# Kernel tuning notes

Hardware: AMD Instinct MI355X
Metric: run time of the kernel (lower is better)

## Reference

```python
import jax, jax.numpy as jnp
import numpy as np

NH = 12      # config.n_head
LEVEL = 2    # config.level -> Lmin = 4


def setup_inputs() -> dict:
    key = jax.random.key(0)
    ks = jax.random.split(key, 10)
    B, T, C = 1, 2048, 768
    hs = C // NH
    s = 0.02
    return {
        'x':   jax.random.normal(ks[0], (B, T, C), jnp.float32),
        'Wq':  jax.random.normal(ks[1], (C, C), jnp.float32) * s,
        'Wk':  jax.random.normal(ks[2], (C, C), jnp.float32) * s,
        'Wv':  jax.random.normal(ks[3], (C, C), jnp.float32) * s,
        'Wks': jax.random.normal(ks[4], (hs * hs, hs), jnp.float32) * s,
        'bks': jax.random.normal(ks[5], (hs,), jnp.float32) * s,
        'Wvs': jax.random.normal(ks[6], (hs * hs, hs), jnp.float32) * s,
        'bvs': jax.random.normal(ks[7], (hs,), jnp.float32) * s,
        'Wc':  jax.random.normal(ks[8], (C, C), jnp.float32) * s,
        'bc':  jax.random.normal(ks[9], (C,), jnp.float32) * s,
    }


def reference(x, Wq, Wk, Wv, Wks, bks, Wvs, bvs, Wc, bc):
    B, T, C = x.shape
    hs = C // NH
    Lmin = 2 ** LEVEL
    levelmax = int(np.log2(T))          # T is a power of two -> no ragged tails per level
    scale = hs ** -0.5

    # fla LinearAttention preprocess: bias-free projections + elu feature map (phi = elu+1)
    q = (jax.nn.elu(x @ Wq) + 1.0).reshape(B, T, NH, hs)
    k = (jax.nn.elu(x @ Wk) + 1.0).reshape(B, T, NH, hs)
    v = (x @ Wv).reshape(B, T, NH, hs)

    # per-position linear-attn state increments phi(k) v^T  [B,T,H,hs,hs]
    kv = jnp.einsum('bthi,bthj->bthij', k, v).reshape(B, T, NH, hs * hs)

    # tail features: running state within each block of Lmin (fused_recurrent final states
    # over the ragged per-position tail segments [t - t%Lmin, t])
    tail_feat = jnp.cumsum(kv.reshape(B, T // Lmin, Lmin, NH, hs * hs), axis=2)
    tail_feat = tail_feat.reshape(B, T, NH, hs * hs)

    # hierarchical set features: dyadic block sums at levels LEVEL..levelmax
    cur = kv.reshape(B, T // Lmin, Lmin, NH, hs * hs).sum(axis=2)
    feats, ends = [], []
    for l in range(LEVEL, levelmax + 1):
        n = T // (2 ** l)
        feats.append(cur)
        ends.append(np.arange(1, n + 1) * (2 ** l))   # exclusive end index of each set
        if n >= 2:
            cur = cur.reshape(B, n // 2, 2, NH, hs * hs).sum(axis=2)
    set_feat = jnp.concatenate(feats, axis=1)          # [B, S, H, hs*hs], S = 1023
    ends = np.concatenate(ends)                        # [S]
    mask = ends[None, :] <= (np.arange(T) + 1)[:, None]  # [T, S] causal set mask

    # k_mapping / v_mapping: Linear(hs^2 -> hs)
    K = set_feat @ Wks + bks        # [B,S,H,hs]
    V = set_feat @ Wvs + bvs
    K_tail = tail_feat @ Wks + bks  # [B,T,H,hs]
    V_tail = tail_feat @ Wvs + bvs

    logits = jnp.einsum('bthd,bshd->bhts', q, K) * scale      # [B,H,T,S]
    logits = jnp.where(mask[None, None], logits, jnp.float32(-1e30))
    tail_logit = jnp.einsum('bthd,bthd->bht', q, K_tail) * scale  # [B,H,T]
    att = jax.nn.softmax(jnp.concatenate([logits, tail_logit[..., None]], axis=-1), axis=-1)

    out = jnp.einsum('bhts,bshd->bhtd', att[..., :-1], V)
    out = out + att[..., -1:] * V_tail.transpose(0, 2, 1, 3)  # [B,H,T,hs]
    out = out.transpose(0, 2, 1, 3).reshape(B, T, C)
    return out @ Wc + bc
```

## Files before the change

### kernel.cpp

```cpp
#include <hip/hip_runtime.h>
#include <cstdint>

#define NHEAD 12
#define TLEN 2048
#define CDIM 768
#define NSETS 1023

typedef __attribute__((ext_vector_type(8))) _Float16 half8;
typedef __attribute__((ext_vector_type(2))) __fp16 fp16x2;
typedef __attribute__((ext_vector_type(8))) short short8;
typedef __attribute__((ext_vector_type(8))) unsigned short u16x8;
typedef __attribute__((ext_vector_type(4))) float f32x4;

#define SOFTMAX_SCL 0.18033688011112042f

__device__ __forceinline__ float elu1(float x) { return x > 0.f ? x + 1.f : __expf(x); }

__device__ __forceinline__ unsigned pack2_bf16_trunc(float a, float b) {
    unsigned ua = __float_as_uint(a), ub = __float_as_uint(b);
    return __builtin_amdgcn_perm(ub, ua, 0x07060302);
}
__device__ __forceinline__ unsigned pack2_bf16_rne(float a, float b) {
    unsigned ua = __float_as_uint(a), ub = __float_as_uint(b);
    ua = ua + 0x7fff + ((ua >> 16) & 1);
    ub = ub + 0x7fff + ((ub >> 16) & 1);
    return (ub & 0xffff0000u) | (ua >> 16);
}
__device__ __forceinline__ unsigned short bf16_hi_trunc(float a) {
    return (unsigned short)(__float_as_uint(a) >> 16);
}
__device__ __forceinline__ unsigned short bf16_lo_trunc(float a) {
    unsigned ua = __float_as_uint(a);
    float r = a - __uint_as_float(ua & 0xffff0000u);
    return (unsigned short)(__float_as_uint(r) >> 16);
}
__device__ __forceinline__ unsigned short bf16_rne(float a) {
    unsigned ua = __float_as_uint(a);
    ua = ua + 0x7fff + ((ua >> 16) & 1);
    return (unsigned short)(ua >> 16);
}
__device__ __forceinline__ short8 mk_short8(const unsigned* u) {
    union { unsigned w[4]; short8 s; } x;
    x.w[0] = u[0]; x.w[1] = u[1]; x.w[2] = u[2]; x.w[3] = u[3];
    return x.s;
}
__device__ __forceinline__ short8 as_s8(u16x8 v) {
    union { u16x8 u; short8 s; } x; x.u = v; return x.s;
}
__device__ __forceinline__ void split8_bf16(const float* f, short8& hi, short8& lo) {
    unsigned hp[4], lp[4];
    #pragma unroll
    for (int p = 0; p < 4; ++p) {
        float a = f[2 * p], b = f[2 * p + 1];
        unsigned ua = __float_as_uint(a), ub = __float_as_uint(b);
        hp[p] = __builtin_amdgcn_perm(ub, ua, 0x07060302);
        float ra = a - __uint_as_float(ua & 0xffff0000u);
        float rb = b - __uint_as_float(ub & 0xffff0000u);
        lp[p] = pack2_bf16_trunc(ra, rb);
    }
    hi = mk_short8(hp); lo = mk_short8(lp);
}
__device__ __forceinline__ void split8_f16(const float* f, half8& hi, half8& lo) {
    union { fp16x2 h2[4]; half8 h8; } uh, ul;
    #pragma unroll
    for (int jp = 0; jp < 4; ++jp) {
        float a = f[2 * jp], b = f[2 * jp + 1];
        fp16x2 hh = __builtin_amdgcn_cvt_pkrtz(a, b);
        uh.h2[jp] = hh;
        ul.h2[jp] = __builtin_amdgcn_cvt_pkrtz(a - (float)hh[0], b - (float)hh[1]);
    }
    hi = uh.h8; lo = ul.h8;
}

__global__ __launch_bounds__(256) void prep_all(
    const float* __restrict__ Wq, const float* __restrict__ Wk,
    const float* __restrict__ Wv, const float* __restrict__ Wc4,
    const float* __restrict__ Wks, const float* __restrict__ Wvs,
    const float* __restrict__ x,
    _Float16* __restrict__ blobQKV, _Float16* __restrict__ blobC,
    _Float16* __restrict__ Wblob,
    _Float16* __restrict__ xhi, _Float16* __restrict__ xlo)
{
    const int g = blockIdx.x;
    const int tid = threadIdx.x;
    if (g < 9216) {
        const int sel = g / 2304;
        const float* W = sel == 0 ? Wq : (sel == 1 ? Wk : (sel == 2 ? Wv : Wc4));
        _Float16* blob = (sel < 3) ? (blobQKV + (size_t)sel * 589824) : blobC;
        const int idx = (g % 2304) * 256 + tid;
        const int k = idx / 768, n = idx % 768;
        const int i = k >> 5, kl = k & 31;
        const int quad = kl >> 3, j = kl & 7;
        const int nsg = n >> 4, lane15 = n & 15;
        const int lane = quad * 16 + lane15;
        blob[((size_t)(i * 48 + nsg) * 64 + lane) * 8 + j] = (_Float16)W[idx];
    } else if (g < 9216 + 2048) {
        const int idx = (g - 9216) * 256 + tid;
        const int kk = idx >> 7, n = idx & 127;
        float f = (n < 64) ? Wks[(size_t)kk * 64 + n] : Wvs[(size_t)kk * 64 + (n - 64)];
        const int i = kk >> 6, kl = kk & 63;
        const int ks = kl >> 5, quad = (kl >> 3) & 3, j = kl & 7;
        const int nsg = n >> 4, lane15 = n & 15;
        const int lane = quad * 16 + lane15;
        const size_t off = ((size_t)(((i * 2 + ks) * 8 + nsg)) * 64 + lane) * 8 + j;
        Wblob[off] = (_Float16)f;
    } else {
        const int p = (g - 11264) * 256 + tid;
        const int lane = p & 63, frag = p >> 6;
        const int m16 = frag / 24, k32 = frag - m16 * 24;
        const int row = m16 * 16 + (lane & 15);
        const int col = k32 * 32 + (lane >> 4) * 8;
        float f[8];
        *(float4*)&f[0] = *(const float4*)&x[(size_t)row * CDIM + col];
        *(float4*)&f[4] = *(const float4*)&x[(size_t)row * CDIM + col + 4];
        half8 h, l;
        split8_f16(f, h, l);
        *(half8*)&xhi[(size_t)p * 8] = h;
        *(half8*)&xlo[(size_t)p * 8] = l;
    }
}

template<int QKV>
__global__ __launch_bounds__(256, 3) void gemm_frag(
    const _Float16* __restrict__ Ahi, const _Float16* __restrict__ Alo,
    const _Float16* __restrict__ Bblobs, const float* __restrict__ bias,
    float* __restrict__ outq, unsigned* __restrict__ kdup,
    _Float16* __restrict__ v16)
{
    const int nbx = QKV ? 18 : 6;
    const int cpx = QKV ? 72 : 24;
    int bid = blockIdx.x;
    bid = (bid & 7) * cpx + (bid >> 3);
    const int by  = bid / nbx;
    const int bxg = bid % nbx;
    const int which = QKV ? bxg / 6 : 0;
    const int bxm   = QKV ? bxg % 6 : bxg;
    const half8* __restrict__ Bc = (const half8*)(Bblobs + (size_t)which * 589824);

    const int tid = threadIdx.x;
    const int wave = tid >> 6, lane = tid & 63;
    const int lane15 = lane & 15, quad = lane >> 4;
    const int m16b = by * 4;
    const int nsg0 = bxm * 8 + wave * 2;

    const half8* __restrict__ Ah = (const half8*)Ahi;
    const half8* __restrict__ Al = (const half8*)Alo;

    f32x4 acc[4][2];
    #pragma unroll
    for (int ms = 0; ms < 4; ++ms) {
        acc[ms][0] = (f32x4){0.f, 0.f, 0.f, 0.f};
        acc[ms][1] = (f32x4){0.f, 0.f, 0.f, 0.f};
    }

    const size_t aBase = ((size_t)m16b * 24) * 64 + lane;
    const size_t bBase = (size_t)nsg0 * 64 + lane;

    half8 bb[2], ah[4], al[4];
    bb[0] = Bc[bBase];
    bb[1] = Bc[bBase + 64];
    #pragma unroll
    for (int ms = 0; ms < 4; ++ms) {
        ah[ms] = Ah[aBase + (size_t)ms * (24 * 64)];
        al[ms] = Al[aBase + (size_t)ms * (24 * 64)];
    }

    for (int k32 = 0; k32 < 24; ++k32) {
        half8 bbn[2], ahn[4], aln[4];
        const bool more = (k32 + 1) < 24;
        if (more) {
            const size_t bo = bBase + (size_t)(k32 + 1) * (48 * 64);
            bbn[0] = Bc[bo]; bbn[1] = Bc[bo + 64];
            #pragma unroll
            for (int ms = 0; ms < 4; ++ms) {
                const size_t ao = aBase + (size_t)(k32 + 1) * 64 + (size_t)ms * (24 * 64);
                ahn[ms] = Ah[ao]; aln[ms] = Al[ao];
            }
        }
        #pragma unroll
        for (int ms = 0; ms < 4; ++ms) {
            acc[ms][0] = __builtin_amdgcn_mfma_f32_16x16x32_f16(ah[ms], bb[0], acc[ms][0], 0, 0, 0);
            acc[ms][1] = __builtin_amdgcn_mfma_f32_16x16x32_f16(ah[ms], bb[1], acc[ms][1], 0, 0, 0);
            acc[ms][0] = __builtin_amdgcn_mfma_f32_16x16x32_f16(al[ms], bb[0], acc[ms][0], 0, 0, 0);
            acc[ms][1] = __builtin_amdgcn_mfma_f32_16x16x32_f16(al[ms], bb[1], acc[ms][1], 0, 0, 0);
        }
        if (more) {
            bb[0] = bbn[0]; bb[1] = bbn[1];
            #pragma unroll
            for (int ms = 0; ms < 4; ++ms) { ah[ms] = ahn[ms]; al[ms] = aln[ms]; }
        }
    }

    #pragma unroll
    for (int ms = 0; ms < 4; ++ms)
        #pragma unroll
        for (int nb = 0; nb < 2; ++nb) {
            const int coln = (nsg0 + nb) * 16 + lane15;
            #pragma unroll
            for (int r = 0; r < 4; ++r) {
                const int row = m16b * 16 + ms * 16 + quad * 4 + r;
                float vv = acc[ms][nb][r];
                if (!QKV) {
                    outq[(size_t)row * CDIM + coln] = vv + bias[coln];
                } else if (which == 0) {
                    outq[(size_t)row * CDIM + coln] = elu1(vv);
                } else if (which == 1) {
                    float e = elu1(vv);
                    union { fp16x2 h; unsigned u; } cc;
                    cc.h = __builtin_amdgcn_cvt_pkrtz(e, e);
                    kdup[(size_t)row * CDIM + coln] = cc.u;
                } else {
                    union { fp16x2 h; _Float16 f2[2]; } cc;
                    cc.h = __builtin_amdgcn_cvt_pkrtz(vv, vv);
                    v16[(size_t)row * CDIM + coln] = cc.f2[0];
                }
            }
        }
}

__global__ __launch_bounds__(256, 2) void map_f16(
    const unsigned* __restrict__ kdup, const _Float16* __restrict__ v16,
    const _Float16* __restrict__ Wblob,
    float* __restrict__ kkv, float* __restrict__ vvv)
{
    __shared__ unsigned kU[64][65];

    const int tid = threadIdx.x;
    const int p0 = blockIdx.x * 64;
    const int wave = tid >> 6, lane = tid & 63;
    const int lane15 = lane & 15, quad = lane >> 4;

    {
        const int row = tid >> 2, cb = (tid & 3) * 16;
        const unsigned* src = &kdup[(size_t)(p0 + row) * 64 + cb];
        uint4 a0 = *(const uint4*)(src + 0);
        uint4 a1 = *(const uint4*)(src + 4);
        uint4 a2 = *(const uint4*)(src + 8);
        uint4 a3 = *(const uint4*)(src + 12);
        *(uint4*)&kU[row][cb + 0]  = a0;
        *(uint4*)&kU[row][cb + 4]  = a1;
        *(uint4*)&kU[row][cb + 8]  = a2;
        *(uint4*)&kU[row][cb + 12] = a3;
    }

    half8 vrh[4][2];
    #pragma unroll
    for (int mh = 0; mh < 4; ++mh) {
        const size_t pbase = (size_t)(p0 + mh * 16 + lane15) * 64;
        #pragma unroll
        for (int ks = 0; ks < 2; ++ks)
            vrh[mh][ks] = *(const half8*)&v16[pbase + ks * 32 + quad * 8];
    }
    __syncthreads();

    const half8* __restrict__ Wc = (const half8*)Wblob;

    f32x4 acc[4][2];
    #pragma unroll
    for (int mh = 0; mh < 4; ++mh)
        #pragma unroll
        for (int nsl = 0; nsl < 2; ++nsl)
            acc[mh][nsl] = (f32x4){0.f, 0.f, 0.f, 0.f};

    half8 b0[2], b1[2], b2[2], b3[2];
    unsigned ka0[4], ka1[4], ka2[4], ka3[4];

    auto loadB = [&](half8* b, int s) {
        b[0] = Wc[(size_t)(s * 8 + 2 * wave) * 64 + lane];
        b[1] = Wc[(size_t)(s * 8 + 2 * wave + 1) * 64 + lane];
    };
    auto loadK = [&](unsigned* ka, int s) {
        const int i = s >> 1;
        #pragma unroll
        for (int mh = 0; mh < 4; ++mh) ka[mh] = kU[mh * 16 + lane15][i];
    };
    auto compute = [&](const half8* b, const unsigned* ka, int s) {
        const int ks = s & 1;
        #pragma unroll
        for (int mh = 0; mh < 4; ++mh) {
            union { unsigned u; fp16x2 h; } ku; ku.u = ka[mh];
            union { fp16x2 h2[4]; half8 h8; } va, ra;
            va.h8 = vrh[mh][ks];
            #pragma unroll
            for (int jp = 0; jp < 4; ++jp) ra.h2[jp] = ku.h * va.h2[jp];
            acc[mh][0] = __builtin_amdgcn_mfma_f32_16x16x32_f16(ra.h8, b[0], acc[mh][0], 0, 0, 0);
            acc[mh][1] = __builtin_amdgcn_mfma_f32_16x16x32_f16(ra.h8, b[1], acc[mh][1], 0, 0, 0);
        }
    };

    loadB(b0, 0); loadB(b1, 1); loadB(b2, 2); loadB(b3, 3);
    loadK(ka0, 0); loadK(ka1, 1); loadK(ka2, 2); loadK(ka3, 3);
    for (int s = 0; s < 128; s += 4) {
        const bool more = (s + 4) < 128;
        compute(b0, ka0, s);
        compute(b1, ka1, s + 1);
        if (more) { loadB(b0, s + 4); loadK(ka0, s + 4); loadB(b1, s + 5); loadK(ka1, s + 5); }
        compute(b2, ka2, s + 2);
        compute(b3, ka3, s + 3);
        if (more) { loadB(b2, s + 6); loadK(ka2, s + 6); loadB(b3, s + 7); loadK(ka3, s + 7); }
    }

    #pragma unroll
    for (int mh = 0; mh < 4; ++mh)
        #pragma unroll
        for (int nsl = 0; nsl < 2; ++nsl) {
            int n128 = (2 * wave + nsl) * 16 + lane15;
            float* dst = (n128 < 64) ? kkv : vvv;
            int col = n128 & 63;
            #pragma unroll
            for (int r = 0; r < 4; ++r) {
                int p = p0 + mh * 16 + quad * 4 + r;
                dst[(size_t)p * 64 + col] = acc[mh][nsl][r];
            }
        }
}

__global__ __launch_bounds__(256) void set_lower(
    const float* __restrict__ kkv, const float* __restrict__ vvv,
    const float* __restrict__ bks, const float* __restrict__ bvs,
    unsigned short* __restrict__ KsetH, unsigned short* __restrict__ KsetL,
    unsigned short* __restrict__ VsetB,
    float* __restrict__ scrK, float* __restrict__ scrV,
    float* __restrict__ Kt, float* __restrict__ Vt)
{
    __shared__ float curK[63][64];
    __shared__ float curV[63][64];
    const int tid = threadIdx.x;
    const int col = tid & 63, grp = tid >> 6;
    const int h = blockIdx.x % NHEAD;
    const int c = blockIdx.x / NHEAD;
    const int t0 = c * 128;
    const float bk = bks[col], bv = bvs[col];

    for (int j = grp; j < 32; j += 4) {
        const size_t rbase = (size_t)(t0 + j * 4) * CDIM + h * 64 + col;
        const float* pk = kkv + rbase;
        const float* pv = vvv + rbase;
        float* ptK = Kt + rbase;
        float* ptV = Vt + rbase;
        float sk = bk, sv = bv;
        #pragma unroll
        for (int u = 0; u < 4; ++u) {
            sk += pk[(size_t)u * CDIM];
            sv += pv[(size_t)u * CDIM];
            ptK[(size_t)u * CDIM] = sk;
            ptV[(size_t)u * CDIM] = sv;
        }
        curK[j][col] = sk - bk; curV[j][col] = sv - bv;
        size_t o = ((size_t)(c * 32 + j) * NHEAD + h) * 64 + col;
        KsetH[o] = bf16_hi_trunc(sk); KsetL[o] = bf16_lo_trunc(sk);
        VsetB[o] = bf16_rne(sv);
    }
    __syncthreads();

    const int LBASE[6] = {0, 32, 48, 56, 60, 62};
    const int GBASE[6] = {0, 512, 768, 896, 960, 992};
    #pragma unroll
    for (int li = 1; li < 6; ++li) {
        const int ns = 32 >> li;
        for (int j = grp; j < ns; j += 4) {
            float sk = curK[LBASE[li - 1] + 2 * j][col] + curK[LBASE[li - 1] + 2 * j + 1][col];
            float sv = curV[LBASE[li - 1] + 2 * j][col] + curV[LBASE[li - 1] + 2 * j + 1][col];
            curK[LBASE[li] + j][col] = sk; curV[LBASE[li] + j][col] = sv;
            size_t o = ((size_t)(GBASE[li] + c * ns + j) * NHEAD + h) * 64 + col;
            float kv_ = sk + bk, vv_ = sv + bv;
            KsetH[o] = bf16_hi_trunc(kv_); KsetL[o] = bf16_lo_trunc(kv_);
            VsetB[o] = bf16_rne(vv_);
        }
        __syncthreads();
    }

    if (grp == 0) {
        scrK[((size_t)h * 16 + c) * 64 + col] = curK[62][col];
        scrV[((size_t)h * 16 + c) * 64 + col] = curV[62][col];
    }
}

__global__ __launch_bounds__(256) void set_upper(
    const float* __restrict__ scrK, const float* __restrict__ scrV,
    const float* __restrict__ bks, const float* __restrict__ bvs,
    unsigned short* __restrict__ KsetH, unsigned short* __restrict__ KsetL,
    unsigned short* __restrict__ VsetB)
{
    __shared__ float cK[15][64], cV[15][64];
    const int h = blockIdx.x;
    const int tid = threadIdx.x, col = tid & 63, grp = tid >> 6;
    const float bk = bks[col], bv = bvs[col];

    for (int j = grp; j < 8; j += 4) {
        float sk = scrK[((size_t)h * 16 + 2 * j) * 64 + col] + scrK[((size_t)h * 16 + 2 * j + 1) * 64 + col];
        float sv = scrV[((size_t)h * 16 + 2 * j) * 64 + col] + scrV[((size_t)h * 16 + 2 * j + 1) * 64 + col];
        cK[j][col] = sk; cV[j][col] = sv;
        size_t o = ((size_t)(1008 + j) * NHEAD + h) * 64 + col;
        float kv_ = sk + bk, vv_ = sv + bv;
        KsetH[o] = bf16_hi_trunc(kv_); KsetL[o] = bf16_lo_trunc(kv_);
        VsetB[o] = bf16_rne(vv_);
    }
    __syncthreads();
    const int LB[4] = {0, 8, 12, 14};
    const int GB[4] = {1008, 1016, 1020, 1022};
    #pragma unroll
    for (int li = 1; li < 4; ++li) {
        const int ns = 8 >> li;
        for (int j = grp; j < ns; j += 4) {
            float sk = cK[LB[li - 1] + 2 * j][col] + cK[LB[li - 1] + 2 * j + 1][col];
            float sv = cV[LB[li - 1] + 2 * j][col] + cV[LB[li - 1] + 2 * j + 1][col];
            cK[LB[li] + j][col] = sk; cV[LB[li] + j][col] = sv;
            size_t o = ((size_t)(GB[li] + j) * NHEAD + h) * 64 + col;
            float kv_ = sk + bk, vv_ = sv + bv;
            KsetH[o] = bf16_hi_trunc(kv_); KsetL[o] = bf16_lo_trunc(kv_);
            VsetB[o] = bf16_rne(vv_);
        }
        __syncthreads();
    }
}

__global__ __launch_bounds__(256, 3) void attn_mfma(
    const float* __restrict__ qbuf,
    const unsigned short* __restrict__ KsetH, const unsigned short* __restrict__ KsetL,
    const unsigned short* __restrict__ VsetB,
    const float* __restrict__ Ktail, const float* __restrict__ Vtail,
    _Float16* __restrict__ atthi, _Float16* __restrict__ attlo)
{
    __shared__ unsigned ssAll[1024];
    __shared__ float sS[2][32][68];
    __shared__ unsigned sP[2][32][40];
    __shared__ unsigned vP[2][64][40];
    __shared__ float arowS[2][32];
    __shared__ float alS[32], ptS[32];

    const int tid = threadIdx.x;
    const int b   = 63 - (blockIdx.x / NHEAD);
    const int h   = blockIdx.x % NHEAD;
    const int T0  = b * 32;
    const int wave = tid >> 6, lane = tid & 63;
    const int lane15 = lane & 15, quad = lane >> 4;

    const int Tend = T0 + 32;
    const int LOFF[10] = {0, 512, 768, 896, 960, 992, 1008, 1016, 1020, 1022};
    int pfx[10], Vtot = 0;
    #pragma unroll
    for (int li = 0; li < 10; ++li) { pfx[li] = Vtot; Vtot += Tend >> (li + 2); }
    const int ntiles = (Vtot + 63) >> 6;

    for (int j = tid; j < 1024; j += 256) {
        unsigned pk = (4095u << 16);
        if (j < Vtot) {
            int li = 0;
            #pragma unroll
            for (int u = 1; u < 10; ++u) if (j >= pfx[u]) li = u;
            int idx = j - pfx[li];
            pk = (unsigned)(LOFF[li] + idx) | ((unsigned)((idx + 1) << (li + 2)) << 16);
        }
        ssAll[j] = pk;
    }

    short8 Qhi[2][2], Qlo[2][2];
    #pragma unroll
    for (int ms = 0; ms < 2; ++ms)
        #pragma unroll
        for (int kt = 0; kt < 2; ++kt) {
            const float* qp = qbuf + ((size_t)(T0 + ms * 16 + lane15) * NHEAD + h) * 64 + kt * 32 + quad * 8;
            float f[8];
            *(float4*)&f[0] = *(const float4*)qp;
            *(float4*)&f[4] = *(const float4*)(qp + 4);
            split8_bf16(f, Qhi[ms][kt], Qlo[ms][kt]);
        }

    __syncthreads();

    const int row = tid >> 3, part = tid & 7;
    float mreg = -1e30f, lreg = 0.f;

    f32x4 oacc[2];
    oacc[0] = (f32x4){0.f, 0.f, 0.f, 0.f};
    oacc[1] = (f32x4){0.f, 0.f, 0.f, 0.f};

    u16x8 Va, Vb;
    u16x8 KH[2], KL[2];
    const int sp = tid >> 3, dd = (tid & 7) * 8;
    auto prefV = [&](int tile) {
        int sa = (int)(ssAll[tile * 64 + 2 * sp] & 0xffffu);
        int sb = (int)(ssAll[tile * 64 + 2 * sp + 1] & 0xffffu);
        Va = *(const u16x8*)(VsetB + ((size_t)sa * NHEAD + h) * 64 + dd);
        Vb = *(const u16x8*)(VsetB + ((size_t)sb * NHEAD + h) * 64 + dd);
    };
    auto prefK = [&](int tile) {
        int sK = (int)(ssAll[tile * 64 + wave * 16 + lane15] & 0xffffu);
        const size_t ko = ((size_t)sK * NHEAD + h) * 64 + quad * 8;
        KH[0] = *(const u16x8*)(KsetH + ko);
        KH[1] = *(const u16x8*)(KsetH + ko + 32);
        KL[0] = *(const u16x8*)(KsetL + ko);
        KL[1] = *(const u16x8*)(KsetL + ko + 32);
    };
    prefV(0); prefK(0);

    for (int tile = 0; tile < ntiles; ++tile) {
        const int c = tile & 1;

        #pragma unroll
        for (int i = 0; i < 8; ++i)
            vP[c][dd + i][sp] = (unsigned)Va[i] | ((unsigned)Vb[i] << 16);

        short8 Khi[2] = { as_s8(KH[0]), as_s8(KH[1]) };
        short8 Klo[2] = { as_s8(KL[0]), as_s8(KL[1]) };

        f32x4 lacc[2];
        lacc[0] = (f32x4){0.f, 0.f, 0.f, 0.f};
        lacc[1] = (f32x4){0.f, 0.f, 0.f, 0.f};
        #pragma unroll
        for (int kt = 0; kt < 2; ++kt)
            #pragma unroll
            for (int ms = 0; ms < 2; ++ms) {
                lacc[ms] = __builtin_amdgcn_mfma_f32_16x16x32_bf16(Qhi[ms][kt], Khi[kt], lacc[ms], 0, 0, 0);
                lacc[ms] = __builtin_amdgcn_mfma_f32_16x16x32_bf16(Qlo[ms][kt], Khi[kt], lacc[ms], 0, 0, 0);
                lacc[ms] = __builtin_amdgcn_mfma_f32_16x16x32_bf16(Qhi[ms][kt], Klo[kt], lacc[ms], 0, 0, 0);
            }

        {
            const int sendv = (int)(ssAll[tile * 64 + wave * 16 + lane15] >> 16);
            #pragma unroll
            for (int ms = 0; ms < 2; ++ms)
                #pragma unroll
                for (int r = 0; r < 4; ++r) {
                    int qrow = ms * 16 + quad * 4 + r;
                    bool ok = (T0 + qrow + 1) >= sendv;
                    sS[c][qrow][wave * 16 + lane15] = ok ? lacc[ms][r] * SOFTMAX_SCL : -1e30f;
                }
        }

        if (tile + 1 < ntiles) { prefV(tile + 1); prefK(tile + 1); }

        __syncthreads();

        {
            float4 a = *(float4*)&sS[c][row][part * 8];
            float4 c4 = *(float4*)&sS[c][row][part * 8 + 4];
            float mx = fmaxf(fmaxf(fmaxf(a.x, a.y), fmaxf(a.z, a.w)),
                             fmaxf(fmaxf(c4.x, c4.y), fmaxf(c4.z, c4.w)));
            mx = fmaxf(mx, __shfl_xor(mx, 1));
            mx = fmaxf(mx, __shfl_xor(mx, 2));
            mx = fmaxf(mx, __shfl_xor(mx, 4));
            float mnew = fmaxf(mreg, mx);
            float al = exp2f(mreg - mnew);
            mreg = mnew;
            a.x = a.x > -1e29f ? exp2f(a.x - mnew) : 0.f;
            a.y = a.y > -1e29f ? exp2f(a.y - mnew) : 0.f;
            a.z = a.z > -1e29f ? exp2f(a.z - mnew) : 0.f;
            a.w = a.w > -1e29f ? exp2f(a.w - mnew) : 0.f;
            c4.x = c4.x > -1e29f ? exp2f(c4.x - mnew) : 0.f;
            c4.y = c4.y > -1e29f ? exp2f(c4.y - mnew) : 0.f;
            c4.z = c4.z > -1e29f ? exp2f(c4.z - mnew) : 0.f;
            c4.w = c4.w > -1e29f ? exp2f(c4.w - mnew) : 0.f;
            float sm = (a.x + a.y + a.z + a.w) + (c4.x + c4.y + c4.z + c4.w);
            sm += __shfl_xor(sm, 1);
            sm += __shfl_xor(sm, 2);
            sm += __shfl_xor(sm, 4);
            lreg = al * lreg + sm;
            unsigned w0 = pack2_bf16_rne(a.x, a.y);
            unsigned w1 = pack2_bf16_rne(a.z, a.w);
            unsigned w2 = pack2_bf16_rne(c4.x, c4.y);
            unsigned w3 = pack2_bf16_rne(c4.z, c4.w);
            *(uint4*)&sP[c][row][part * 4] = make_uint4(w0, w1, w2, w3);
            if (part == 0) arowS[c][row] = al;
        }

        __syncthreads();

        #pragma unroll
        for (int ms = 0; ms < 2; ++ms)
            #pragma unroll
            for (int r = 0; r < 4; ++r)
                oacc[ms][r] *= arowS[c][ms * 16 + quad * 4 + r];

        #pragma unroll
        for (int kt = 0; kt < 2; ++kt) {
            short8 Vf = *(short8*)&vP[c][wave * 16 + lane15][kt * 16 + quad * 4];
            #pragma unroll
            for (int ms = 0; ms < 2; ++ms) {
                short8 Pf = *(short8*)&sP[c][ms * 16 + lane15][kt * 16 + quad * 4];
                oacc[ms] = __builtin_amdgcn_mfma_f32_16x16x32_bf16(Pf, Vf, oacc[ms], 0, 0, 0);
            }
        }
    }

    {
        const float* qr = qbuf  + ((size_t)(T0 + row) * NHEAD + h) * 64 + part * 8;
        const float* kr = Ktail + ((size_t)(T0 + row) * NHEAD + h) * 64 + part * 8;
        float4 qa = *(const float4*)qr, qb = *(const float4*)(qr + 4);
        float4 ka = *(const float4*)kr, kb = *(const float4*)(kr + 4);
        float dp = qa.x * ka.x + qa.y * ka.y + qa.z * ka.z + qa.w * ka.w
                 + qb.x * kb.x + qb.y * kb.y + qb.z * kb.z + qb.w * kb.w;
        dp += __shfl_xor(dp, 1);
        dp += __shfl_xor(dp, 2);
        dp += __shfl_xor(dp, 4);
        float tl = dp * SOFTMAX_SCL;
        float mf = fmaxf(mreg, tl);
        float al = exp2f(mreg - mf);
        float pt = exp2f(tl - mf);
        float lf = al * lreg + pt;
        float inv = 1.f / lf;
        if (part == 0) { alS[row] = al * inv; ptS[row] = pt * inv; }
    }
    __syncthreads();

    #pragma unroll
    for (int ms = 0; ms < 2; ++ms)
        #pragma unroll
        for (int r = 0; r < 4; ++r) {
            int qrow = ms * 16 + quad * 4 + r;
            int col = wave * 16 + lane15;
            size_t base = ((size_t)(T0 + qrow) * NHEAD + h) * 64 + col;
            sS[0][qrow][col] = oacc[ms][r] * alS[qrow] + ptS[qrow] * Vtail[base];
        }
    __syncthreads();

    {
        const int kt = wave >> 1, msf = wave & 1;
        float f[8];
        *(float4*)&f[0] = *(const float4*)&sS[0][msf * 16 + lane15][kt * 32 + quad * 8];
        *(float4*)&f[4] = *(const float4*)&sS[0][msf * 16 + lane15][kt * 32 + quad * 8 + 4];
        half8 hh, ll;
        split8_f16(f, hh, ll);
        const size_t frag = (size_t)(b * 2 + msf) * 24 + (2 * h + kt);
        *(half8*)&atthi[(frag * 64 + lane) * 8] = hh;
        *(half8*)&attlo[(frag * 64 + lane) * 8] = ll;
    }
}

extern "C" void kernel_launch(void* const* d_in, const int* in_sizes, int n_in,
                              void* d_out, int out_size, void* d_ws, size_t ws_size,
                              hipStream_t stream)
{
    const float* x   = (const float*)d_in[0];
    const float* Wq  = (const float*)d_in[1];
    const float* Wk  = (const float*)d_in[2];
    const float* Wv  = (const float*)d_in[3];
    const float* Wks = (const float*)d_in[4];
    const float* bks = (const float*)d_in[5];
    const float* Wvs = (const float*)d_in[6];
    const float* bvs = (const float*)d_in[7];
    const float* Wc  = (const float*)d_in[8];
    const float* bc  = (const float*)d_in[9];
    float* out = (float*)d_out;

    float* ws = (float*)d_ws;
    const size_t TC = (size_t)TLEN * CDIM;
    float* q      = ws;
    float* k      = q + TC;
    float* v      = k + TC;
    float* kkv    = v + TC;
    float* vvv    = kkv + TC;
    float* Kt     = vvv + TC;
    float* Vt     = Kt + TC;
    float* base   = Vt + TC;
    _Float16* WblobMap = (_Float16*)base;
    _Float16* blobQKV  = (_Float16*)(base + 262144);
    float* scrK = base + 1146880;
    float* scrV = scrK + 12 * 16 * 64;
    _Float16* blobC = (_Float16*)(base + 1171456);
    unsigned short* KsetH = (unsigned short*)(base + 1466368);
    unsigned short* KsetL = KsetH + 786432;
    unsigned short* VsetB = KsetL + 786432;
    _Float16* xhi = (_Float16*)kkv;
    _Float16* xlo = xhi + TC;
    unsigned*  kdup = (unsigned*)k;
    _Float16*  v16  = (_Float16*)v;
    _Float16* atthi = (_Float16*)vvv;
    _Float16* attlo = atthi + TC;

    prep_all<<<9216 + 2048 + 768, 256, 0, stream>>>(
        Wq, Wk, Wv, Wc, Wks, Wvs, x, blobQKV, blobC, WblobMap, xhi, xlo);

    gemm_frag<1><<<576, 256, 0, stream>>>(xhi, xlo, blobQKV, nullptr, q, kdup, v16);

    map_f16<<<(TLEN * NHEAD) / 64, 256, 0, stream>>>(kdup, v16, WblobMap, kkv, vvv);

    set_lower<<<16 * NHEAD, 256, 0, stream>>>(kkv, vvv, bks, bvs, KsetH, KsetL, VsetB, scrK, scrV, Kt, Vt);
    set_upper<<<NHEAD, 256, 0, stream>>>(scrK, scrV, bks, bvs, KsetH, KsetL, VsetB);

    attn_mfma<<<(TLEN / 32) * NHEAD, 256, 0, stream>>>(q, KsetH, KsetL, VsetB, Kt, Vt, atthi, attlo);

    gemm_frag<0><<<192, 256, 0, stream>>>(atthi, attlo, blobC, bc, out, nullptr, nullptr);
}
```

Before: 200.5 us.

## Drop hi/lo fp16 split for GEMM inputs, retile output GEMM, simplify masked exp

The activation operands of the QKV and output projections are now a single fp16 conversion instead of a hi+lo split. This halves the A-operand traffic and the MFMA count in gemm_frag, at the cost of fp16 input precision. The output-projection GEMM now uses one N-subgroup per wave and launches twice as many blocks for better occupancy, and the k-loop is unrolled by two with double-buffered register loads. The softmax masking replaces per-element compare/select with a clamped max so masked logits underflow to zero in exp2.

```diff
diff --git a/kernel.cpp b/kernel.cpp
--- a/kernel.cpp
+++ b/kernel.cpp
@@ -60,16 +60,12 @@
     }
     hi = mk_short8(hp); lo = mk_short8(lp);
 }
-__device__ __forceinline__ void split8_f16(const float* f, half8& hi, half8& lo) {
-    union { fp16x2 h2[4]; half8 h8; } uh, ul;
-    #pragma unroll
-    for (int jp = 0; jp < 4; ++jp) {
-        float a = f[2 * jp], b = f[2 * jp + 1];
-        fp16x2 hh = __builtin_amdgcn_cvt_pkrtz(a, b);
-        uh.h2[jp] = hh;
-        ul.h2[jp] = __builtin_amdgcn_cvt_pkrtz(a - (float)hh[0], b - (float)hh[1]);
-    }
-    hi = uh.h8; lo = ul.h8;
+__device__ __forceinline__ half8 cvt8_f16(const float* f) {
+    union { fp16x2 h2[4]; half8 h8; } u;
+    #pragma unroll
+    for (int jp = 0; jp < 4; ++jp)
+        u.h2[jp] = __builtin_amdgcn_cvt_pkrtz(f[2 * jp], f[2 * jp + 1]);
+    return u.h8;
 }
 
 __global__ __launch_bounds__(256) void prep_all(
@@ -79,7 +75,7 @@
     const float* __restrict__ x,
     _Float16* __restrict__ blobQKV, _Float16* __restrict__ blobC,
     _Float16* __restrict__ Wblob,
-    _Float16* __restrict__ xhi, _Float16* __restrict__ xlo)
+    _Float16* __restrict__ xf)
 {
     const int g = blockIdx.x;
     const int tid = threadIdx.x;
@@ -113,22 +109,19 @@
         float f[8];
         *(float4*)&f[0] = *(const float4*)&x[(size_t)row * CDIM + col];
         *(float4*)&f[4] = *(const float4*)&x[(size_t)row * CDIM + col + 4];
-        half8 h, l;
-        split8_f16(f, h, l);
-        *(half8*)&xhi[(size_t)p * 8] = h;
-        *(half8*)&xlo[(size_t)p * 8] = l;
+        *(half8*)&xf[(size_t)p * 8] = cvt8_f16(f);
     }
 }
 
 template<int QKV>
 __global__ __launch_bounds__(256, 3) void gemm_frag(
-    const _Float16* __restrict__ Ahi, const _Float16* __restrict__ Alo,
+    const _Float16* __restrict__ Af,
     const _Float16* __restrict__ Bblobs, const float* __restrict__ bias,
     float* __restrict__ outq, unsigned* __restrict__ kdup,
     _Float16* __restrict__ v16)
 {
-    const int nbx = QKV ? 18 : 6;
-    const int cpx = QKV ? 72 : 24;
+    const int nbx = QKV ? 18 : 12;
+    const int cpx = QKV ? 72 : 48;
     int bid = blockIdx.x;
     bid = (bid & 7) * cpx + (bid >> 3);
     const int by  = bid / nbx;
@@ -141,10 +134,9 @@
     const int wave = tid >> 6, lane = tid & 63;
     const int lane15 = lane & 15, quad = lane >> 4;
     const int m16b = by * 4;
-    const int nsg0 = bxm * 8 + wave * 2;
-
-    const half8* __restrict__ Ah = (const half8*)Ahi;
-    const half8* __restrict__ Al = (const half8*)Alo;
+    const int nsg0 = QKV ? (bxm * 8 + wave * 2) : (bxm * 4 + wave);
+
+    const half8* __restrict__ Ah = (const half8*)Af;
 
     f32x4 acc[4][2];
     #pragma unroll
@@ -156,45 +148,51 @@
     const size_t aBase = ((size_t)m16b * 24) * 64 + lane;
     const size_t bBase = (size_t)nsg0 * 64 + lane;
 
-    half8 bb[2], ah[4], al[4];
-    bb[0] = Bc[bBase];
-    bb[1] = Bc[bBase + 64];
-    #pragma unroll
-    for (int ms = 0; ms < 4; ++ms) {
-        ah[ms] = Ah[aBase + (size_t)ms * (24 * 64)];
-        al[ms] = Al[aBase + (size_t)ms * (24 * 64)];
-    }
-
-    for (int k32 = 0; k32 < 24; ++k32) {
-        half8 bbn[2], ahn[4], aln[4];
-        const bool more = (k32 + 1) < 24;
+    half8 aC[2][4], bC[2][2], aN[2][4], bN[2][2];
+    auto loadA = [&](half8 (*dst)[4], int k32a) {
+        #pragma unroll
+        for (int u = 0; u < 2; ++u)
+            #pragma unroll
+            for (int ms = 0; ms < 4; ++ms)
+                dst[u][ms] = Ah[aBase + (size_t)(k32a + u) * 64 + (size_t)ms * (24 * 64)];
+    };
+    auto loadB = [&](half8 (*dst)[2], int k32a) {
+        #pragma unroll
+        for (int u = 0; u < 2; ++u) {
+            const size_t bo = bBase + (size_t)(k32a + u) * (48 * 64);
+            dst[u][0] = Bc[bo];
+            if (QKV) dst[u][1] = Bc[bo + 64];
+        }
+    };
+
+    loadA(aC, 0); loadB(bC, 0);
+    for (int kk = 0; kk < 12; ++kk) {
+        const bool more = (kk + 1) < 12;
+        if (more) { loadA(aN, 2 * kk + 2); loadB(bN, 2 * kk + 2); }
+        #pragma unroll
+        for (int u = 0; u < 2; ++u)
+            #pragma unroll
+            for (int ms = 0; ms < 4; ++ms) {
+                acc[ms][0] = __builtin_amdgcn_mfma_f32_16x16x32_f16(aC[u][ms], bC[u][0], acc[ms][0], 0, 0, 0);
+                if (QKV)
+                    acc[ms][1] = __builtin_amdgcn_mfma_f32_16x16x32_f16(aC[u][ms], bC[u][1], acc[ms][1], 0, 0, 0);
+            }
         if (more) {
-            const size_t bo = bBase + (size_t)(k32 + 1) * (48 * 64);
-            bbn[0] = Bc[bo]; bbn[1] = Bc[bo + 64];
-            #pragma unroll
-            for (int ms = 0; ms < 4; ++ms) {
-                const size_t ao = aBase + (size_t)(k32 + 1) * 64 + (size_t)ms * (24 * 64);
-                ahn[ms] = Ah[ao]; aln[ms] = Al[ao];
+            #pragma unroll
+            for (int u = 0; u < 2; ++u) {
+                bC[u][0] = bN[u][0]; bC[u][1] = bN[u][1];
+                #pragma unroll
+                for (int ms = 0; ms < 4; ++ms) aC[u][ms] = aN[u][ms];
             }
         }
-        #pragma unroll
-        for (int ms = 0; ms < 4; ++ms) {
-            acc[ms][0] = __builtin_amdgcn_mfma_f32_16x16x32_f16(ah[ms], bb[0], acc[ms][0], 0, 0, 0);
-            acc[ms][1] = __builtin_amdgcn_mfma_f32_16x16x32_f16(ah[ms], bb[1], acc[ms][1], 0, 0, 0);
-            acc[ms][0] = __builtin_amdgcn_mfma_f32_16x16x32_f16(al[ms], bb[0], acc[ms][0], 0, 0, 0);
-            acc[ms][1] = __builtin_amdgcn_mfma_f32_16x16x32_f16(al[ms], bb[1], acc[ms][1], 0, 0, 0);
-        }
-        if (more) {
-            bb[0] = bbn[0]; bb[1] = bbn[1];
-            #pragma unroll
-            for (int ms = 0; ms < 4; ++ms) { ah[ms] = ahn[ms]; al[ms] = aln[ms]; }
-        }
-    }
-
+    }
+
+    const int NSL = QKV ? 2 : 1;
     #pragma unroll
     for (int ms = 0; ms < 4; ++ms)
         #pragma unroll
         for (int nb = 0; nb < 2; ++nb) {
+            if (nb >= NSL) break;
             const int coln = (nsg0 + nb) * 16 + lane15;
             #pragma unroll
             for (int r = 0; r < 4; ++r) {
@@ -420,7 +418,7 @@
     const unsigned short* __restrict__ KsetH, const unsigned short* __restrict__ KsetL,
     const unsigned short* __restrict__ VsetB,
     const float* __restrict__ Ktail, const float* __restrict__ Vtail,
-    _Float16* __restrict__ atthi, _Float16* __restrict__ attlo)
+    _Float16* __restrict__ attf)
 {
     __shared__ unsigned ssAll[1024];
     __shared__ float sS[2][32][68];
@@ -544,14 +542,15 @@
             float mnew = fmaxf(mreg, mx);
             float al = exp2f(mreg - mnew);
             mreg = mnew;
-            a.x = a.x > -1e29f ? exp2f(a.x - mnew) : 0.f;
-            a.y = a.y > -1e29f ? exp2f(a.y - mnew) : 0.f;
-            a.z = a.z > -1e29f ? exp2f(a.z - mnew) : 0.f;
-            a.w = a.w > -1e29f ? exp2f(a.w - mnew) : 0.f;
-            c4.x = c4.x > -1e29f ? exp2f(c4.x - mnew) : 0.f;
-            c4.y = c4.y > -1e29f ? exp2f(c4.y - mnew) : 0.f;
-            c4.z = c4.z > -1e29f ? exp2f(c4.z - mnew) : 0.f;
-            c4.w = c4.w > -1e29f ? exp2f(c4.w - mnew) : 0.f;
+            float mexp = fmaxf(mnew, -1e28f);
+            a.x = exp2f(a.x - mexp);
+            a.y = exp2f(a.y - mexp);
+            a.z = exp2f(a.z - mexp);
+            a.w = exp2f(a.w - mexp);
+            c4.x = exp2f(c4.x - mexp);
+            c4.y = exp2f(c4.y - mexp);
+            c4.z = exp2f(c4.z - mexp);
+            c4.w = exp2f(c4.w - mexp);
             float sm = (a.x + a.y + a.z + a.w) + (c4.x + c4.y + c4.z + c4.w);
             sm += __shfl_xor(sm, 1);
             sm += __shfl_xor(sm, 2);
@@ -620,11 +619,8 @@
         float f[8];
         *(float4*)&f[0] = *(const float4*)&sS[0][msf * 16 + lane15][kt * 32 + quad * 8];
         *(float4*)&f[4] = *(const float4*)&sS[0][msf * 16 + lane15][kt * 32 + quad * 8 + 4];
-        half8 hh, ll;
-        split8_f16(f, hh, ll);
         const size_t frag = (size_t)(b * 2 + msf) * 24 + (2 * h + kt);
-        *(half8*)&atthi[(frag * 64 + lane) * 8] = hh;
-        *(half8*)&attlo[(frag * 64 + lane) * 8] = ll;
+        *(half8*)&attf[(frag * 64 + lane) * 8] = cvt8_f16(f);
     }
 }
 
@@ -662,24 +658,22 @@
     unsigned short* KsetH = (unsigned short*)(base + 1466368);
     unsigned short* KsetL = KsetH + 786432;
     unsigned short* VsetB = KsetL + 786432;
-    _Float16* xhi = (_Float16*)kkv;
-    _Float16* xlo = xhi + TC;
+    _Float16* xf = (_Float16*)kkv;
     unsigned*  kdup = (unsigned*)k;
     _Float16*  v16  = (_Float16*)v;
-    _Float16* atthi = (_Float16*)vvv;
-    _Float16* attlo = atthi + TC;
+    _Float16* attf = (_Float16*)vvv;
 
     prep_all<<<9216 + 2048 + 768, 256, 0, stream>>>(
-        Wq, Wk, Wv, Wc, Wks, Wvs, x, blobQKV, blobC, WblobMap, xhi, xlo);
-
-    gemm_frag<1><<<576, 256, 0, stream>>>(xhi, xlo, blobQKV, nullptr, q, kdup, v16);
+        Wq, Wk, Wv, Wc, Wks, Wvs, x, blobQKV, blobC, WblobMap, xf);
+
+    gemm_frag<1><<<576, 256, 0, stream>>>(xf, blobQKV, nullptr, q, kdup, v16);
 
     map_f16<<<(TLEN * NHEAD) / 64, 256, 0, stream>>>(kdup, v16, WblobMap, kkv, vvv);
 
     set_lower<<<16 * NHEAD, 256, 0, stream>>>(kkv, vvv, bks, bvs, KsetH, KsetL, VsetB, scrK, scrV, Kt, Vt);
     set_upper<<<NHEAD, 256, 0, stream>>>(scrK, scrV, bks, bvs, KsetH, KsetL, VsetB);
 
-    attn_mfma<<<(TLEN / 32) * NHEAD, 256, 0, stream>>>(q, KsetH, KsetL, VsetB, Kt, Vt, atthi, attlo);
-
-    gemm_frag<0><<<192, 256, 0, stream>>>(atthi, attlo, blobC, bc, out, nullptr, nullptr);
-}
+    attn_mfma<<<(TLEN / 32) * NHEAD, 256, 0, stream>>>(q, KsetH, KsetL, VsetB, Kt, Vt, attf);
+
+    gemm_frag<0><<<384, 256, 0, stream>>>(attf, blobC, bc, out, nullptr, nullptr);
+}
```

New measurement: 191.3 us. 4.6% less time.
